# Optimization experiments

Measured on AMD Instinct MI355X. Metric: run time of the kernel, lower is better.

## Reference

```python
import jax, jax.numpy as jnp
import numpy as np
import math

EMBED_DIM = 1024
NUM_HEADS = 16
HEAD_DIM = EMBED_DIM // NUM_HEADS
ACT_BITS = 8
WGT_BITS = 8


def fake_quant(x, n_bits):
    # Per-tensor symmetric fake quantization with straight-through estimator.
    qmax = 2.0 ** (n_bits - 1) - 1.0  # 127 for 8 bits
    scale = jnp.maximum(jnp.max(jnp.abs(x)) / qmax, 1e-8)
    q = jnp.clip(jnp.round(x / scale), -qmax - 1.0, qmax) * scale
    return x + jax.lax.stop_gradient(q - x)


def setup_inputs() -> dict:
    key = jax.random.key(0)
    ks = jax.random.split(key, 7)
    S, B, D = 2048, 2, EMBED_DIM
    return {
        "query": jax.random.normal(ks[0], (S, B, D), dtype=jnp.float32),
        "key": jax.random.normal(ks[1], (S, B, D), dtype=jnp.float32),
        "value": jax.random.normal(ks[2], (S, B, D), dtype=jnp.float32),
        "Wi": jax.random.normal(ks[3], (3 * D, D), dtype=jnp.float32) * (1.0 / math.sqrt(D)),
        "bi": jax.random.normal(ks[4], (3 * D,), dtype=jnp.float32) * 0.01,
        "Wo": jax.random.normal(ks[5], (D, D), dtype=jnp.float32) * (1.0 / math.sqrt(D)),
        "bo": jax.random.normal(ks[6], (D,), dtype=jnp.float32) * 0.01,
    }


def reference(query, key, value, Wi, bi, Wo, bo):
    D, H, hd = EMBED_DIM, NUM_HEADS, HEAD_DIM
    len_q, batch, _ = query.shape
    len_k = key.shape[0]

    Wi_q = fake_quant(Wi, WGT_BITS)
    Wo_q = fake_quant(Wo, WGT_BITS)

    # in-projections (full 3D projection per input, then chunk, as in source)
    Xq = fake_quant(query @ Wi_q.T + bi, ACT_BITS)
    Xk = fake_quant(key @ Wi_q.T + bi, ACT_BITS)
    Xv = fake_quant(value @ Wi_q.T + bi, ACT_BITS)
    Q = Xq[..., :D]
    K = Xk[..., D:2 * D]
    V = Xv[..., 2 * D:]

    # [len, B, D] -> [B*H, len, hd]
    q = Q.reshape(len_q, batch * H, hd).transpose(1, 0, 2)
    k = K.reshape(len_k, batch * H, hd).transpose(1, 0, 2)
    v = V.reshape(len_k, batch * H, hd).transpose(1, 0, 2)

    q = fake_quant(q / math.sqrt(hd), ACT_BITS)
    attn = jnp.einsum('bqd,bkd->bqk', q, k)  # note: attn/softmax fake-quants in source are no-ops (result discarded)
    attn = jax.nn.softmax(attn, axis=-1)
    heads = fake_quant(jnp.einsum('bqk,bkd->bqd', attn, v), ACT_BITS)

    # [B*H, len_q, hd] -> [len_q*B, D]
    heads_reshape = heads.transpose(1, 0, 2).reshape(len_q * batch, D)
    y = (heads_reshape @ Wo_q.T + bo).reshape(len_q, batch, D)
    return fake_quant(y, ACT_BITS)
```

## Files before the change

kernel.cpp:

```cpp
#include <hip/hip_runtime.h>
#include <math.h>


typedef _Float16 f16;
typedef _Float16 half8 __attribute__((ext_vector_type(8)));
typedef _Float16 half4 __attribute__((ext_vector_type(4)));
typedef _Float16 half2v __attribute__((ext_vector_type(2)));
typedef __fp16 fp16x2 __attribute__((ext_vector_type(2)));
typedef float floatx4 __attribute__((ext_vector_type(4)));
typedef int int4v __attribute__((ext_vector_type(4)));

#define QMAX 127.0f

#define SLOT_WI 0
#define SLOT_WO 1
#define SLOT_XQ 2
#define SLOT_XK 3
#define SLOT_XV 4
#define SLOT_HD 5
#define SLOT_Y  6
#define SLOT_Q  7
#define SLOT_A  8

__device__ __forceinline__ float slot_scale(const unsigned* slots, int slot, float premul) {
  if (slot < 0) return 1.0f;
  return fmaxf(__uint_as_float(slots[slot]) * premul / QMAX, 1e-8f);
}

__device__ __forceinline__ float slot_scaleA(const unsigned* slots) {
  return fmaxf(__uint_as_float(slots[SLOT_A]) / 16256.0f, 1e-8f);
}

__device__ __forceinline__ void gl2lds16(const void* gsrc, void* ldst) {
  __builtin_amdgcn_global_load_lds((__attribute__((address_space(1))) void*)gsrc,
                                   (__attribute__((address_space(3))) void*)ldst, 16, 0, 0);
}

__device__ __forceinline__ half2v pack2(float a, float b) {
  fp16x2 r = __builtin_amdgcn_cvt_pkrtz(a, b);
  return __builtin_bit_cast(half2v, r);
}


__global__ __launch_bounds__(256) void absmax3_k(const float* __restrict__ Wi,
                                                 const float* __restrict__ Wo,
                                                 const float* __restrict__ q,
                                                 const float* __restrict__ k,
                                                 const float* __restrict__ v,
                                                 unsigned* __restrict__ slots) {
  __shared__ float red[256];
  int tid = threadIdx.x;
  int bid = blockIdx.x;
  const float4* x4;
  int n4, i0, stride, slot;
  if (bid < 768) {
    x4 = (const float4*)Wi; n4 = 786432; i0 = bid * 256 + tid;
    stride = 768 * 256; slot = SLOT_WI;
  } else if (bid < 1024) {
    x4 = (const float4*)Wo; n4 = 262144; i0 = (bid - 768) * 256 + tid;
    stride = 256 * 256; slot = SLOT_WO;
  } else {
    int r = bid - 1024;
    int t = r >> 9;
    x4 = (const float4*)(t == 0 ? q : (t == 1 ? k : v));
    n4 = 1048576; i0 = (r & 511) * 256 + tid;
    stride = 512 * 256; slot = SLOT_A;
  }
  float lmax = 0.f;
  for (int i = i0; i < n4; i += stride) {
    float4 vv = x4[i];
    lmax = fmaxf(lmax, fmaxf(fmaxf(fabsf(vv.x), fabsf(vv.y)), fmaxf(fabsf(vv.z), fabsf(vv.w))));
  }
  red[tid] = lmax; __syncthreads();
  for (int sh = 128; sh > 0; sh >>= 1) {
    if (tid < sh) red[tid] = fmaxf(red[tid], red[tid + sh]);
    __syncthreads();
  }
  if (tid == 0) atomicMax(&slots[slot], __float_as_uint(red[0]));
}

__global__ __launch_bounds__(256) void quantw_k(const float* __restrict__ Wi,
                                                const float* __restrict__ Wo,
                                                char* __restrict__ Wi8,
                                                char* __restrict__ Wo8,
                                                const unsigned* __restrict__ slots) {
  int j = blockIdx.x * 256 + threadIdx.x;
  const float* src; char* dst; float s; int a;
  if (j < 196608) {
    s = slot_scale(slots, SLOT_WI, 1.0f); src = Wi; dst = Wi8; a = j;
  } else {
    s = slot_scale(slots, SLOT_WO, 1.0f); src = Wo; dst = Wo8; a = j - 196608;
  }
  int m = ((a >> 10) << 4) | (a & 15);
  int k0 = ((((a >> 6) & 15) << 2) | ((a >> 4) & 3)) << 4;
  const float4* row = (const float4*)(src + (size_t)m * 1024 + k0);
  char ob[16] __attribute__((aligned(16)));
#pragma unroll
  for (int c = 0; c < 4; ++c) {
    float4 x = row[c];
    float xs[4] = {x.x, x.y, x.z, x.w};
#pragma unroll
    for (int u = 0; u < 4; ++u)
      ob[c * 4 + u] = (signed char)(int)fminf(fmaxf(rintf(xs[u] / s), -128.0f), 127.0f);
  }
  *(int4*)(dst + (size_t)a * 16) = *(const int4*)ob;
}

__global__ __launch_bounds__(256) void digitize_k(const float* __restrict__ q,
                                                  const float* __restrict__ k,
                                                  const float* __restrict__ v,
                                                  char* __restrict__ A1,
                                                  char* __restrict__ A2,
                                                  const unsigned* __restrict__ slots) {
  float inv = 1.0f / slot_scaleA(slots);
  int j = blockIdx.x * 256 + threadIdx.x;
  int t = j >> 18;
  int a = j & 262143;
  const float* src = (t == 0 ? q : (t == 1 ? k : v));
  int m = ((a >> 10) << 4) | (a & 15);
  int k0 = ((((a >> 6) & 15) << 2) | ((a >> 4) & 3)) << 4;
  const float4* row = (const float4*)(src + (size_t)m * 1024 + k0);
  char o1[16] __attribute__((aligned(16)));
  char o2[16] __attribute__((aligned(16)));
#pragma unroll
  for (int c = 0; c < 4; ++c) {
    float4 x = row[c];
    float xs[4] = {x.x, x.y, x.z, x.w};
#pragma unroll
    for (int u = 0; u < 4; ++u) {
      float qv = fminf(fmaxf(rintf(xs[u] * inv), -16256.0f), 16256.0f);
      float c1 = rintf(qv * 0.0078125f);
      o1[c * 4 + u] = (signed char)(int)c1;
      o2[c * 4 + u] = (signed char)(int)(qv - 128.0f * c1);
    }
  }
  size_t off = (size_t)t * 4194304 + (size_t)a * 16;
  *(int4*)(A1 + off) = *(const int4*)o1;
  *(int4*)(A2 + off) = *(const int4*)o2;
}

__global__ __launch_bounds__(256) void quantf_k(const float* __restrict__ in, float* __restrict__ out,
                                                int n4, unsigned* __restrict__ slots,
                                                int sSlot, float premul) {
  float s = slot_scale(slots, sSlot, premul);
  const float4* in4 = (const float4*)in;
  float4* out4 = (float4*)out;
  for (int i = blockIdx.x * 256 + threadIdx.x; i < n4; i += gridDim.x * 256) {
    float4 v = in4[i];
    float xs[4] = {v.x, v.y, v.z, v.w};
#pragma unroll
    for (int u = 0; u < 4; ++u) {
      float r = rintf((xs[u] * premul) / s);
      r = fminf(fmaxf(r, -128.0f), 127.0f);
      xs[u] = r * s;
    }
    out4[i] = make_float4(xs[0], xs[1], xs[2], xs[3]);
  }
}

__global__ __launch_bounds__(256) void quanti2_k(const float* __restrict__ Xk,
                                                 f16* __restrict__ Kint,
                                                 const float* __restrict__ Xq,
                                                 f16* __restrict__ Qc,
                                                 unsigned* __restrict__ slots) {
  __shared__ float red[256];
  bool isQ = blockIdx.x >= 1024;
  const float* in = isQ ? Xq : Xk;
  f16* out = isQ ? Qc : Kint;
  float s = slot_scale(slots, isQ ? SLOT_XQ : SLOT_XK, 1.0f);
  int b = isQ ? blockIdx.x - 1024 : blockIdx.x;
  float lmax = 0.f;
  const float4* in4 = (const float4*)in;
  for (int i = b * 256 + threadIdx.x; i < 1048576; i += 1024 * 256) {
    float4 v = in4[i];
    float xs[4] = {v.x, v.y, v.z, v.w};
    half4 o;
#pragma unroll
    for (int u = 0; u < 4; ++u) {
      float r = rintf(xs[u] / s);
      r = fminf(fmaxf(r, -128.0f), 127.0f);
      o[u] = (f16)r;
      lmax = fmaxf(lmax, fabsf(r));
    }
    *(half4*)(out + (size_t)i * 4) = o;
  }
  if (isQ) {
    int tid = threadIdx.x;
    red[tid] = lmax; __syncthreads();
    for (int sh = 128; sh > 0; sh >>= 1) {
      if (tid < sh) red[tid] = fmaxf(red[tid], red[tid + sh]);
      __syncthreads();
    }
    if (tid == 0) atomicMax(&slots[SLOT_Q], __float_as_uint(red[0] * s));
  }
}

__global__ __launch_bounds__(256) void quant8_k(const float* __restrict__ in, char* __restrict__ out,
                                                const unsigned* __restrict__ slots,
                                                int sSlot) {
  float s = slot_scale(slots, sSlot, 1.0f);
  int a = blockIdx.x * 256 + threadIdx.x;
  int m = ((a >> 10) << 4) | (a & 15);
  int k0 = ((((a >> 6) & 15) << 2) | ((a >> 4) & 3)) << 4;
  const float4* row = (const float4*)(in + (size_t)m * 1024 + k0);
  char ob[16] __attribute__((aligned(16)));
#pragma unroll
  for (int c = 0; c < 4; ++c) {
    float4 x = row[c];
    float xs[4] = {x.x, x.y, x.z, x.w};
#pragma unroll
    for (int u = 0; u < 4; ++u)
      ob[c * 4 + u] = (signed char)(int)fminf(fmaxf(rintf(xs[u] / s), -128.0f), 127.0f);
  }
  *(int4*)(out + (size_t)a * 16) = *(const int4*)ob;
}

__global__ __launch_bounds__(256) void quantv_t_k(const float* __restrict__ Xv,
                                                  f16* __restrict__ Vt,
                                                  const unsigned* __restrict__ slots) {
  __shared__ f16 T[64][68];
  int tid = threadIdx.x;
  int bh = blockIdx.y, b = bh >> 4, h = bh & 15;
  int k0 = blockIdx.x * 64;
  float s = slot_scale(slots, SLOT_XV, 1.0f);
#pragma unroll
  for (int it = 0; it < 4; ++it) {
    int idx = tid + it * 256;
    int row = idx >> 4, dseg = idx & 15;
    float4 v = *(const float4*)(Xv + ((size_t)(k0 + row) * 2 + b) * 1024 + h * 64 + dseg * 4);
    float xs[4] = {v.x, v.y, v.z, v.w};
    half4 o;
#pragma unroll
    for (int u = 0; u < 4; ++u) {
      float r = rintf(xs[u] / s);
      o[u] = (f16)fminf(fmaxf(r, -128.0f), 127.0f);
    }
    *(half4*)&T[row][dseg * 4] = o;
  }
  __syncthreads();
#pragma unroll
  for (int it = 0; it < 2; ++it) {
    int sdx = tid + it * 256;
    int d = sdx >> 3, j8 = sdx & 7;
    half8 o;
#pragma unroll
    for (int l = 0; l < 8; ++l) {
      int pos = j8 * 8 + l;
      int tp = pos >> 5, pq = (pos & 31) >> 3, jj = pos & 7;
      int k = tp * 32 + pq * 4 + ((jj < 4) ? jj : jj + 12);
      o[l] = T[k][d];
    }
    *(half8*)(Vt + ((size_t)bh * 64 + d) * 2048 + k0 + j8 * 8) = o;
  }
}

__global__ __launch_bounds__(512) void gemm_qkv_i8_k(const char* __restrict__ A1,
                                                     const char* __restrict__ A2,
                                                     const char* __restrict__ B8,
                                                     const float* __restrict__ bias,
                                                     float* __restrict__ Xout,
                                                     unsigned* __restrict__ slots) {
  __shared__ char As1[2][8192];
  __shared__ char As2[2][8192];
  __shared__ char Bs8[2][8192];
  float* red = (float*)&As1[0][0];

  int tid = threadIdx.x;
  int lane = tid & 63, w = tid >> 6;
  int wm = w >> 1, wn = w & 1;
  int quad = lane >> 4, l15 = lane & 15;
  int t = blockIdx.y >> 5;
  int m0 = (blockIdx.y & 31) * 128;
  int n0 = blockIdx.x * 128;
  size_t aoff = (size_t)t * 4194304;

  const char* a1p = A1 + aoff;
  const char* a2p = A2 + aoff;

  int4v acc1[2][4], acc2[2][4];
#pragma unroll
  for (int i = 0; i < 2; ++i)
#pragma unroll
    for (int j = 0; j < 4; ++j) {
      acc1[i][j] = (int4v){0, 0, 0, 0};
      acc2[i][j] = (int4v){0, 0, 0, 0};
    }

  auto stage = [&](int buf, int kk) __attribute__((always_inline)) {
    size_t ac = ((size_t)((m0 >> 4) + w) << 14) + ((kk >> 6) << 10) + lane * 16;
    size_t bc = ((size_t)((n0 >> 4) + w) << 14) + ((kk >> 6) << 10) + lane * 16;
    gl2lds16(a1p + ac, &As1[buf][w * 1024]);
    gl2lds16(a2p + ac, &As2[buf][w * 1024]);
    gl2lds16(B8 + bc, &Bs8[buf][w * 1024]);
  };

  auto compute = [&](int buf) __attribute__((always_inline)) {
    int4v bf[4];
#pragma unroll
    for (int j = 0; j < 4; ++j)
      bf[j] = *(const int4v*)&Bs8[buf][(wn * 4 + j) * 1024 + lane * 16];
    int4v a1f[2];
#pragma unroll
    for (int i = 0; i < 2; ++i)
      a1f[i] = *(const int4v*)&As1[buf][(wm * 2 + i) * 1024 + lane * 16];
#pragma unroll
    for (int i = 0; i < 2; ++i)
#pragma unroll
      for (int j = 0; j < 4; ++j)
        acc1[i][j] = __builtin_amdgcn_mfma_i32_16x16x64_i8(a1f[i], bf[j], acc1[i][j], 0, 0, 0);
    int4v a2f[2];
#pragma unroll
    for (int i = 0; i < 2; ++i)
      a2f[i] = *(const int4v*)&As2[buf][(wm * 2 + i) * 1024 + lane * 16];
#pragma unroll
    for (int i = 0; i < 2; ++i)
#pragma unroll
      for (int j = 0; j < 4; ++j)
        acc2[i][j] = __builtin_amdgcn_mfma_i32_16x16x64_i8(a2f[i], bf[j], acc2[i][j], 0, 0, 0);
  };

  stage(0, 0);
  __syncthreads();
  for (int kt = 0; kt < 7; ++kt) {
    stage(1, (2 * kt + 1) * 64);
    compute(0);
    __syncthreads();
    stage(0, (2 * kt + 2) * 64);
    compute(1);
    __syncthreads();
  }
  stage(1, 960);
  compute(0);
  __syncthreads();
  compute(1);

  float sc = slot_scaleA(slots) * slot_scale(slots, SLOT_WI, 1.0f);
  int colLo = t * 1024;
  float* outT = Xout + aoff;
  float lmax = 0.f;
#pragma unroll
  for (int i = 0; i < 2; ++i) {
#pragma unroll
    for (int j = 0; j < 4; ++j) {
      int gn = n0 + wn * 64 + j * 16 + l15;
      float bv = bias[gn];
      bool wr = (gn >= colLo && gn < colLo + 1024);
#pragma unroll
      for (int r = 0; r < 4; ++r) {
        int gm = m0 + wm * 32 + i * 16 + quad * 4 + r;
        float vv = fmaf((float)acc1[i][j][r], 128.0f, (float)acc2[i][j][r]) * sc + bv;
        lmax = fmaxf(lmax, fabsf(vv));
        if (wr) outT[(size_t)gm * 1024 + (gn - colLo)] = vv;
      }
    }
  }
  red[tid] = lmax; __syncthreads();
  for (int sh = 256; sh > 0; sh >>= 1) {
    if (tid < sh) red[tid] = fmaxf(red[tid], red[tid + sh]);
    __syncthreads();
  }
  if (tid == 0) atomicMax(&slots[SLOT_XQ + t], __float_as_uint(red[0]));
}

__global__ __launch_bounds__(512) void gemm_i8out_k(const char* __restrict__ A8,
                                                    const char* __restrict__ B8,
                                                    const float* __restrict__ bias,
                                                    float* __restrict__ out,
                                                    unsigned* __restrict__ slots) {
  __shared__ char As8[2][8192];
  __shared__ char Bs8[2][8192];
  float* red = (float*)&As8[0][0];

  int tid = threadIdx.x;
  int lane = tid & 63, w = tid >> 6;
  int wm = w >> 1, wn = w & 1;
  int quad = lane >> 4, l15 = lane & 15;
  int m0 = blockIdx.y * 128, n0 = blockIdx.x * 128;

  int4v acc[2][4];
#pragma unroll
  for (int i = 0; i < 2; ++i)
#pragma unroll
    for (int j = 0; j < 4; ++j) acc[i][j] = (int4v){0, 0, 0, 0};

  auto stage = [&](int buf, int kk) __attribute__((always_inline)) {
    size_t ac = ((size_t)((m0 >> 4) + w) << 14) + ((kk >> 6) << 10) + lane * 16;
    size_t bc = ((size_t)((n0 >> 4) + w) << 14) + ((kk >> 6) << 10) + lane * 16;
    gl2lds16(A8 + ac, &As8[buf][w * 1024]);
    gl2lds16(B8 + bc, &Bs8[buf][w * 1024]);
  };

  auto compute = [&](int buf) __attribute__((always_inline)) {
    int4v bf[4];
#pragma unroll
    for (int j = 0; j < 4; ++j)
      bf[j] = *(const int4v*)&Bs8[buf][(wn * 4 + j) * 1024 + lane * 16];
    int4v af[2];
#pragma unroll
    for (int i = 0; i < 2; ++i)
      af[i] = *(const int4v*)&As8[buf][(wm * 2 + i) * 1024 + lane * 16];
#pragma unroll
    for (int i = 0; i < 2; ++i)
#pragma unroll
      for (int j = 0; j < 4; ++j)
        acc[i][j] = __builtin_amdgcn_mfma_i32_16x16x64_i8(af[i], bf[j], acc[i][j], 0, 0, 0);
  };

  stage(0, 0);
  __syncthreads();
  for (int kt = 0; kt < 7; ++kt) {
    stage(1, (2 * kt + 1) * 64);
    compute(0);
    __syncthreads();
    stage(0, (2 * kt + 2) * 64);
    compute(1);
    __syncthreads();
  }
  stage(1, 960);
  compute(0);
  __syncthreads();
  compute(1);

  float sc = slot_scale(slots, SLOT_HD, 1.0f) * slot_scale(slots, SLOT_WO, 1.0f);
  float lmax = 0.f;
#pragma unroll
  for (int i = 0; i < 2; ++i) {
#pragma unroll
    for (int j = 0; j < 4; ++j) {
      int gn = n0 + wn * 64 + j * 16 + l15;
      float bv = bias[gn];
#pragma unroll
      for (int r = 0; r < 4; ++r) {
        int gm = m0 + wm * 32 + i * 16 + quad * 4 + r;
        float v = (float)acc[i][j][r] * sc + bv;
        lmax = fmaxf(lmax, fabsf(v));
        out[(size_t)gm * 1024 + gn] = v;
      }
    }
  }
  red[tid] = lmax; __syncthreads();
  for (int sh = 256; sh > 0; sh >>= 1) {
    if (tid < sh) red[tid] = fmaxf(red[tid], red[tid + sh]);
    __syncthreads();
  }
  if (tid == 0) atomicMax(&slots[SLOT_Y], __float_as_uint(red[0]));
}

__global__ __launch_bounds__(256) void attn_k(const f16* __restrict__ Qc,
                                              const f16* __restrict__ Kh,
                                              const f16* __restrict__ Vt,
                                              float* __restrict__ heads,
                                              unsigned* __restrict__ slots) {
  __shared__ f16 Ks[2][64 * 64];
  __shared__ f16 Vs[2][64][72];
  __shared__ float lred[4][2][16];
  __shared__ float red[256];

  int tid = threadIdx.x;
  int lane = tid & 63, w = tid >> 6;
  int quad = lane >> 4, l15 = lane & 15;
  int bh = blockIdx.y, b = bh >> 4, h = bh & 15;
  int q0 = blockIdx.x * 128;

  float s1 = slot_scale(slots, SLOT_XQ, 1.0f);
  float sq = slot_scale(slots, SLOT_Q, 0.125f);
  float sk = slot_scale(slots, SLOT_XK, 1.0f);
  float sv = slot_scale(slots, SLOT_XV, 1.0f);
  float cS = sq * sk * 1.44269504088896340736f;
  const float FOFF = 12.0f;

  half8 qf[2][2];
#pragma unroll
  for (int s = 0; s < 2; ++s) {
    const f16* qrow = Qc + ((size_t)(q0 + w * 32 + s * 16 + l15) * 2 + b) * 1024 + h * 64;
    half8 qr0 = *(const half8*)(qrow + quad * 8);
    half8 qr1 = *(const half8*)(qrow + 32 + quad * 8);
#pragma unroll
    for (int u = 0; u < 8; ++u) {
      float x0 = ((float)qr0[u] * s1) * 0.125f;
      float x1 = ((float)qr1[u] * s1) * 0.125f;
      qf[s][0][u] = (f16)fminf(fmaxf(rintf(x0 / sq), -128.0f), 127.0f);
      qf[s][1][u] = (f16)fminf(fmaxf(rintf(x1 / sq), -128.0f), 127.0f);
    }
  }

  int ksrow = lane >> 3;
  int ksp = lane & 7;
  int vr0 = tid >> 3, vs0 = (tid & 7) * 8;

  floatx4 oacc[2][4];
#pragma unroll
  for (int s = 0; s < 2; ++s)
#pragma unroll
    for (int d = 0; d < 4; ++d) oacc[s][d] = (floatx4){0.f, 0.f, 0.f, 0.f};
  float lsum[2] = {0.f, 0.f};

  const f16* vbase = Vt + (size_t)bh * 131072;
  half8 va, vb;

  auto stageK = [&](int bf, int kt) __attribute__((always_inline)) {
#pragma unroll
    for (int t = 0; t < 2; ++t) {
      int r0 = (w * 2 + t) * 8;
      int row = r0 + ksrow;
      int g = ksp ^ (row & 7);
      gl2lds16(Kh + ((size_t)(kt + row) * 2 + b) * 1024 + h * 64 + g * 8, &Ks[bf][r0 * 64]);
    }
  };
  auto loadV = [&](int kt) __attribute__((always_inline)) {
    va = *(const half8*)(vbase + (size_t)vr0 * 2048 + kt + vs0);
    vb = *(const half8*)(vbase + (size_t)(vr0 + 32) * 2048 + kt + vs0);
  };
  auto writeV = [&](int bf) __attribute__((always_inline)) {
    *(half8*)&Vs[bf][vr0][vs0] = va;
    *(half8*)&Vs[bf][vr0 + 32][vs0] = vb;
  };

  auto compute = [&](int bf) __attribute__((always_inline)) {
    half8 aph[2][2], apl[2][2];
#pragma unroll
    for (int t = 0; t < 4; ++t) {
      int row = t * 16 + l15;
      int g1 = quad ^ (row & 7);
      half8 kf0 = *(half8*)&Ks[bf][row * 64 + g1 * 8];
      half8 kf1 = *(half8*)&Ks[bf][row * 64 + (g1 ^ 4) * 8];
      int tp = t >> 1, hi = (t & 1) * 4;
#pragma unroll
      for (int s = 0; s < 2; ++s) {
        floatx4 sacc = (floatx4){0.f, 0.f, 0.f, 0.f};
        sacc = __builtin_amdgcn_mfma_f32_16x16x32_f16(kf0, qf[s][0], sacc, 0, 0, 0);
        sacc = __builtin_amdgcn_mfma_f32_16x16x32_f16(kf1, qf[s][1], sacc, 0, 0, 0);
        float p0 = __builtin_amdgcn_exp2f(fmaf(sacc[0], cS, -FOFF));
        float p1 = __builtin_amdgcn_exp2f(fmaf(sacc[1], cS, -FOFF));
        float p2 = __builtin_amdgcn_exp2f(fmaf(sacc[2], cS, -FOFF));
        float p3 = __builtin_amdgcn_exp2f(fmaf(sacc[3], cS, -FOFF));
        lsum[s] += (p0 + p1) + (p2 + p3);
        half2v h01 = pack2(p0, p1);
        half2v h23 = pack2(p2, p3);
        half2v l01 = pack2(p0 - (float)h01[0], p1 - (float)h01[1]);
        half2v l23 = pack2(p2 - (float)h23[0], p3 - (float)h23[1]);
        aph[s][tp][hi + 0] = h01[0]; aph[s][tp][hi + 1] = h01[1];
        aph[s][tp][hi + 2] = h23[0]; aph[s][tp][hi + 3] = h23[1];
        apl[s][tp][hi + 0] = l01[0]; apl[s][tp][hi + 1] = l01[1];
        apl[s][tp][hi + 2] = l23[0]; apl[s][tp][hi + 3] = l23[1];
      }
    }

#pragma unroll
    for (int d = 0; d < 4; ++d) {
      const f16* vsrow = &Vs[bf][d * 16 + l15][0];
      half8 b0 = *(const half8*)(vsrow + quad * 8);
      half8 b1 = *(const half8*)(vsrow + 32 + quad * 8);
#pragma unroll
      for (int s = 0; s < 2; ++s) {
        oacc[s][d] = __builtin_amdgcn_mfma_f32_16x16x32_f16(aph[s][0], b0, oacc[s][d], 0, 0, 0);
        oacc[s][d] = __builtin_amdgcn_mfma_f32_16x16x32_f16(apl[s][0], b0, oacc[s][d], 0, 0, 0);
        oacc[s][d] = __builtin_amdgcn_mfma_f32_16x16x32_f16(aph[s][1], b1, oacc[s][d], 0, 0, 0);
        oacc[s][d] = __builtin_amdgcn_mfma_f32_16x16x32_f16(apl[s][1], b1, oacc[s][d], 0, 0, 0);
      }
    }
  };

  stageK(0, 0);
  loadV(0);
  writeV(0);
  loadV(64);
  __syncthreads();

  int buf = 0;
  for (int it = 0; it < 31; ++it) {
    stageK(buf ^ 1, (it + 1) * 64);
    writeV(buf ^ 1);
    if (it < 30) loadV((it + 2) * 64);
    compute(buf);
    __syncthreads();
    buf ^= 1;
  }
  compute(buf);

#pragma unroll
  for (int s = 0; s < 2; ++s) {
    float l = lsum[s];
    l += __shfl_xor(l, 16);
    l += __shfl_xor(l, 32);
    lred[w][s][l15] = l;
  }
  float linv[2][4];
#pragma unroll
  for (int s = 0; s < 2; ++s)
#pragma unroll
    for (int r = 0; r < 4; ++r) linv[s][r] = sv / lred[w][s][quad * 4 + r];

  float lmax = 0.f;
#pragma unroll
  for (int s = 0; s < 2; ++s)
#pragma unroll
    for (int d = 0; d < 4; ++d)
#pragma unroll
      for (int r = 0; r < 4; ++r) {
        float hv = oacc[s][d][r] * linv[s][r];
        heads[((size_t)(q0 + w * 32 + s * 16 + quad * 4 + r) * 2 + b) * 1024 +
              h * 64 + d * 16 + l15] = hv;
        lmax = fmaxf(lmax, fabsf(hv));
      }
  red[tid] = lmax; __syncthreads();
  for (int sh = 128; sh > 0; sh >>= 1) {
    if (tid < sh) red[tid] = fmaxf(red[tid], red[tid + sh]);
    __syncthreads();
  }
  if (tid == 0) atomicMax(&slots[SLOT_HD], __float_as_uint(red[0]));
}

extern "C" void kernel_launch(void* const* d_in, const int* in_sizes, int n_in,
                              void* d_out, int out_size, void* d_ws, size_t ws_size,
                              hipStream_t stream) {
  (void)in_sizes; (void)n_in; (void)out_size; (void)ws_size;
  const float* query = (const float*)d_in[0];
  const float* key   = (const float*)d_in[1];
  const float* value = (const float*)d_in[2];
  const float* Wi    = (const float*)d_in[3];
  const float* bi    = (const float*)d_in[4];
  const float* Wo    = (const float*)d_in[5];
  const float* bo    = (const float*)d_in[6];
  float* out = (float*)d_out;

  char* p = (char*)d_ws;
  unsigned* slots = (unsigned*)p;            p += 1024;
  char* Wi8 = p;                             p += 3072 * 1024;
  char* Wo8 = p;                             p += 1024 * 1024;
  char* A1  = p;                             p += 12288 * 1024;
  char* A2  = p;                             p += 12288 * 1024;
  float* Hd = (float*)A1;
  f16* Kint = (f16*)(A2 + 4194304);
  float* Xq = (float*)p;                     p += 4096 * 1024 * 4;
  float* Y  = Xq;
  float* Xk = (float*)p;                     p += 4096 * 1024 * 4;
  f16* Qc   = (f16*)Xk;
  float* Xv = (float*)p;                     p += 4096 * 1024 * 4;
  char* Hint8 = (char*)Xv + 4096 * 1024 * 2;
  f16* Vt   = (f16*)p;                       p += 4096 * 1024 * 2;

  hipMemsetAsync(slots, 0, 64, stream);
  absmax3_k<<<2560, 256, 0, stream>>>(Wi, Wo, query, key, value, slots);
  quantw_k<<<1024, 256, 0, stream>>>(Wi, Wo, Wi8, Wo8, slots);
  digitize_k<<<3072, 256, 0, stream>>>(query, key, value, A1, A2, slots);

  dim3 gq(24, 96);
  gemm_qkv_i8_k<<<gq, 512, 0, stream>>>(A1, A2, Wi8, bi, Xq, slots);

  quanti2_k<<<2048, 256, 0, stream>>>(Xk, Kint, Xq, Qc, slots);

  dim3 gvt(32, 32);
  quantv_t_k<<<gvt, 256, 0, stream>>>(Xv, Vt, slots);

  dim3 ga(16, 32);
  attn_k<<<ga, 256, 0, stream>>>(Qc, Kint, Vt, Hd, slots);

  quant8_k<<<1024, 256, 0, stream>>>(Hd, Hint8, slots, SLOT_HD);

  dim3 g2(8, 32);
  gemm_i8out_k<<<g2, 512, 0, stream>>>(Hint8, Wo8, bo, Y, slots);

  quantf_k<<<1024, 256, 0, stream>>>(Y, out, 1048576, slots, SLOT_Y, 1.0f);
}
```

Baseline: 359.1 us.

## Merge elementwise prep/post kernels and load GEMM B fragments directly from global

```diff
diff --git a/kernel.cpp b/kernel.cpp
--- a/kernel.cpp
+++ b/kernel.cpp
@@ -79,64 +79,65 @@
   if (tid == 0) atomicMax(&slots[slot], __float_as_uint(red[0]));
 }
 
-__global__ __launch_bounds__(256) void quantw_k(const float* __restrict__ Wi,
-                                                const float* __restrict__ Wo,
-                                                char* __restrict__ Wi8,
-                                                char* __restrict__ Wo8,
-                                                const unsigned* __restrict__ slots) {
-  int j = blockIdx.x * 256 + threadIdx.x;
-  const float* src; char* dst; float s; int a;
-  if (j < 196608) {
-    s = slot_scale(slots, SLOT_WI, 1.0f); src = Wi; dst = Wi8; a = j;
+__global__ __launch_bounds__(256) void prep_k(const float* __restrict__ Wi,
+                                              const float* __restrict__ Wo,
+                                              const float* __restrict__ q,
+                                              const float* __restrict__ k,
+                                              const float* __restrict__ v,
+                                              char* __restrict__ Wi8,
+                                              char* __restrict__ Wo8,
+                                              char* __restrict__ A1,
+                                              char* __restrict__ A2,
+                                              const unsigned* __restrict__ slots) {
+  int bid = blockIdx.x;
+  if (bid < 1024) {
+    int j = bid * 256 + threadIdx.x;
+    const float* src; char* dst; float s; int a;
+    if (j < 196608) {
+      s = slot_scale(slots, SLOT_WI, 1.0f); src = Wi; dst = Wi8; a = j;
+    } else {
+      s = slot_scale(slots, SLOT_WO, 1.0f); src = Wo; dst = Wo8; a = j - 196608;
+    }
+    int m = ((a >> 10) << 4) | (a & 15);
+    int k0 = ((((a >> 6) & 15) << 2) | ((a >> 4) & 3)) << 4;
+    const float4* row = (const float4*)(src + (size_t)m * 1024 + k0);
+    char ob[16] __attribute__((aligned(16)));
+#pragma unroll
+    for (int c = 0; c < 4; ++c) {
+      float4 x = row[c];
+      float xs[4] = {x.x, x.y, x.z, x.w};
+#pragma unroll
+      for (int u = 0; u < 4; ++u)
+        ob[c * 4 + u] = (signed char)(int)fminf(fmaxf(rintf(xs[u] / s), -128.0f), 127.0f);
+    }
+    *(int4*)(dst + (size_t)a * 16) = *(const int4*)ob;
   } else {
-    s = slot_scale(slots, SLOT_WO, 1.0f); src = Wo; dst = Wo8; a = j - 196608;
-  }
-  int m = ((a >> 10) << 4) | (a & 15);
-  int k0 = ((((a >> 6) & 15) << 2) | ((a >> 4) & 3)) << 4;
-  const float4* row = (const float4*)(src + (size_t)m * 1024 + k0);
-  char ob[16] __attribute__((aligned(16)));
-#pragma unroll
-  for (int c = 0; c < 4; ++c) {
-    float4 x = row[c];
-    float xs[4] = {x.x, x.y, x.z, x.w};
-#pragma unroll
-    for (int u = 0; u < 4; ++u)
-      ob[c * 4 + u] = (signed char)(int)fminf(fmaxf(rintf(xs[u] / s), -128.0f), 127.0f);
-  }
-  *(int4*)(dst + (size_t)a * 16) = *(const int4*)ob;
-}
-
-__global__ __launch_bounds__(256) void digitize_k(const float* __restrict__ q,
-                                                  const float* __restrict__ k,
-                                                  const float* __restrict__ v,
-                                                  char* __restrict__ A1,
-                                                  char* __restrict__ A2,
-                                                  const unsigned* __restrict__ slots) {
-  float inv = 1.0f / slot_scaleA(slots);
-  int j = blockIdx.x * 256 + threadIdx.x;
-  int t = j >> 18;
-  int a = j & 262143;
-  const float* src = (t == 0 ? q : (t == 1 ? k : v));
-  int m = ((a >> 10) << 4) | (a & 15);
-  int k0 = ((((a >> 6) & 15) << 2) | ((a >> 4) & 3)) << 4;
-  const float4* row = (const float4*)(src + (size_t)m * 1024 + k0);
-  char o1[16] __attribute__((aligned(16)));
-  char o2[16] __attribute__((aligned(16)));
-#pragma unroll
-  for (int c = 0; c < 4; ++c) {
-    float4 x = row[c];
-    float xs[4] = {x.x, x.y, x.z, x.w};
-#pragma unroll
-    for (int u = 0; u < 4; ++u) {
-      float qv = fminf(fmaxf(rintf(xs[u] * inv), -16256.0f), 16256.0f);
-      float c1 = rintf(qv * 0.0078125f);
-      o1[c * 4 + u] = (signed char)(int)c1;
-      o2[c * 4 + u] = (signed char)(int)(qv - 128.0f * c1);
-    }
-  }
-  size_t off = (size_t)t * 4194304 + (size_t)a * 16;
-  *(int4*)(A1 + off) = *(const int4*)o1;
-  *(int4*)(A2 + off) = *(const int4*)o2;
+    float inv = 1.0f / slot_scaleA(slots);
+    int j = (bid - 1024) * 256 + threadIdx.x;
+    int t = j >> 18;
+    int a = j & 262143;
+    const float* src = (t == 0 ? q : (t == 1 ? k : v));
+    int m = ((a >> 10) << 4) | (a & 15);
+    int k0 = ((((a >> 6) & 15) << 2) | ((a >> 4) & 3)) << 4;
+    const float4* row = (const float4*)(src + (size_t)m * 1024 + k0);
+    char o1[16] __attribute__((aligned(16)));
+    char o2[16] __attribute__((aligned(16)));
+#pragma unroll
+    for (int c = 0; c < 4; ++c) {
+      float4 x = row[c];
+      float xs[4] = {x.x, x.y, x.z, x.w};
+#pragma unroll
+      for (int u = 0; u < 4; ++u) {
+        float qv = fminf(fmaxf(rintf(xs[u] * inv), -16256.0f), 16256.0f);
+        float c1 = rintf(qv * 0.0078125f);
+        o1[c * 4 + u] = (signed char)(int)c1;
+        o2[c * 4 + u] = (signed char)(int)(qv - 128.0f * c1);
+      }
+    }
+    size_t off = (size_t)t * 4194304 + (size_t)a * 16;
+    *(int4*)(A1 + off) = *(const int4*)o1;
+    *(int4*)(A2 + off) = *(const int4*)o2;
+  }
 }
 
 __global__ __launch_bounds__(256) void quantf_k(const float* __restrict__ in, float* __restrict__ out,
@@ -158,40 +159,80 @@
   }
 }
 
-__global__ __launch_bounds__(256) void quanti2_k(const float* __restrict__ Xk,
-                                                 f16* __restrict__ Kint,
-                                                 const float* __restrict__ Xq,
-                                                 f16* __restrict__ Qc,
-                                                 unsigned* __restrict__ slots) {
+__global__ __launch_bounds__(256) void post_k(const float* __restrict__ Xk,
+                                              f16* __restrict__ Kint,
+                                              const float* __restrict__ Xq,
+                                              f16* __restrict__ Qc,
+                                              const float* __restrict__ Xv,
+                                              f16* __restrict__ Vt,
+                                              unsigned* __restrict__ slots) {
   __shared__ float red[256];
-  bool isQ = blockIdx.x >= 1024;
-  const float* in = isQ ? Xq : Xk;
-  f16* out = isQ ? Qc : Kint;
-  float s = slot_scale(slots, isQ ? SLOT_XQ : SLOT_XK, 1.0f);
-  int b = isQ ? blockIdx.x - 1024 : blockIdx.x;
-  float lmax = 0.f;
-  const float4* in4 = (const float4*)in;
-  for (int i = b * 256 + threadIdx.x; i < 1048576; i += 1024 * 256) {
-    float4 v = in4[i];
-    float xs[4] = {v.x, v.y, v.z, v.w};
-    half4 o;
-#pragma unroll
-    for (int u = 0; u < 4; ++u) {
-      float r = rintf(xs[u] / s);
-      r = fminf(fmaxf(r, -128.0f), 127.0f);
-      o[u] = (f16)r;
-      lmax = fmaxf(lmax, fabsf(r));
-    }
-    *(half4*)(out + (size_t)i * 4) = o;
-  }
-  if (isQ) {
-    int tid = threadIdx.x;
-    red[tid] = lmax; __syncthreads();
-    for (int sh = 128; sh > 0; sh >>= 1) {
-      if (tid < sh) red[tid] = fmaxf(red[tid], red[tid + sh]);
-      __syncthreads();
-    }
-    if (tid == 0) atomicMax(&slots[SLOT_Q], __float_as_uint(red[0] * s));
+  __shared__ f16 T[64][68];
+  int tid = threadIdx.x;
+  int bid = blockIdx.x;
+  if (bid < 2048) {
+    bool isQ = bid >= 1024;
+    const float* in = isQ ? Xq : Xk;
+    f16* out = isQ ? Qc : Kint;
+    float s = slot_scale(slots, isQ ? SLOT_XQ : SLOT_XK, 1.0f);
+    int b = isQ ? bid - 1024 : bid;
+    float lmax = 0.f;
+    const float4* in4 = (const float4*)in;
+    for (int i = b * 256 + tid; i < 1048576; i += 1024 * 256) {
+      float4 v = in4[i];
+      float xs[4] = {v.x, v.y, v.z, v.w};
+      half4 o;
+#pragma unroll
+      for (int u = 0; u < 4; ++u) {
+        float r = rintf(xs[u] / s);
+        r = fminf(fmaxf(r, -128.0f), 127.0f);
+        o[u] = (f16)r;
+        lmax = fmaxf(lmax, fabsf(r));
+      }
+      *(half4*)(out + (size_t)i * 4) = o;
+    }
+    if (isQ) {
+      red[tid] = lmax; __syncthreads();
+      for (int sh = 128; sh > 0; sh >>= 1) {
+        if (tid < sh) red[tid] = fmaxf(red[tid], red[tid + sh]);
+        __syncthreads();
+      }
+      if (tid == 0) atomicMax(&slots[SLOT_Q], __float_as_uint(red[0] * s));
+    }
+  } else {
+    int vt = bid - 2048;
+    int bh = vt >> 5, b = bh >> 4, h = bh & 15;
+    int k0 = (vt & 31) * 64;
+    float s = slot_scale(slots, SLOT_XV, 1.0f);
+#pragma unroll
+    for (int it = 0; it < 4; ++it) {
+      int idx = tid + it * 256;
+      int row = idx >> 4, dseg = idx & 15;
+      float4 v = *(const float4*)(Xv + ((size_t)(k0 + row) * 2 + b) * 1024 + h * 64 + dseg * 4);
+      float xs[4] = {v.x, v.y, v.z, v.w};
+      half4 o;
+#pragma unroll
+      for (int u = 0; u < 4; ++u) {
+        float r = rintf(xs[u] / s);
+        o[u] = (f16)fminf(fmaxf(r, -128.0f), 127.0f);
+      }
+      *(half4*)&T[row][dseg * 4] = o;
+    }
+    __syncthreads();
+#pragma unroll
+    for (int it = 0; it < 2; ++it) {
+      int sdx = tid + it * 256;
+      int d = sdx >> 3, j8 = sdx & 7;
+      half8 o;
+#pragma unroll
+      for (int l = 0; l < 8; ++l) {
+        int pos = j8 * 8 + l;
+        int tp = pos >> 5, pq = (pos & 31) >> 3, jj = pos & 7;
+        int k = tp * 32 + pq * 4 + ((jj < 4) ? jj : jj + 12);
+        o[l] = T[k][d];
+      }
+      *(half8*)(Vt + ((size_t)bh * 64 + d) * 2048 + k0 + j8 * 8) = o;
+    }
   }
 }
 
@@ -215,45 +256,6 @@
   *(int4*)(out + (size_t)a * 16) = *(const int4*)ob;
 }
 
-__global__ __launch_bounds__(256) void quantv_t_k(const float* __restrict__ Xv,
-                                                  f16* __restrict__ Vt,
-                                                  const unsigned* __restrict__ slots) {
-  __shared__ f16 T[64][68];
-  int tid = threadIdx.x;
-  int bh = blockIdx.y, b = bh >> 4, h = bh & 15;
-  int k0 = blockIdx.x * 64;
-  float s = slot_scale(slots, SLOT_XV, 1.0f);
-#pragma unroll
-  for (int it = 0; it < 4; ++it) {
-    int idx = tid + it * 256;
-    int row = idx >> 4, dseg = idx & 15;
-    float4 v = *(const float4*)(Xv + ((size_t)(k0 + row) * 2 + b) * 1024 + h * 64 + dseg * 4);
-    float xs[4] = {v.x, v.y, v.z, v.w};
-    half4 o;
-#pragma unroll
-    for (int u = 0; u < 4; ++u) {
-      float r = rintf(xs[u] / s);
-      o[u] = (f16)fminf(fmaxf(r, -128.0f), 127.0f);
-    }
-    *(half4*)&T[row][dseg * 4] = o;
-  }
-  __syncthreads();
-#pragma unroll
-  for (int it = 0; it < 2; ++it) {
-    int sdx = tid + it * 256;
-    int d = sdx >> 3, j8 = sdx & 7;
-    half8 o;
-#pragma unroll
-    for (int l = 0; l < 8; ++l) {
-      int pos = j8 * 8 + l;
-      int tp = pos >> 5, pq = (pos & 31) >> 3, jj = pos & 7;
-      int k = tp * 32 + pq * 4 + ((jj < 4) ? jj : jj + 12);
-      o[l] = T[k][d];
-    }
-    *(half8*)(Vt + ((size_t)bh * 64 + d) * 2048 + k0 + j8 * 8) = o;
-  }
-}
-
 __global__ __launch_bounds__(512) void gemm_qkv_i8_k(const char* __restrict__ A1,
                                                      const char* __restrict__ A2,
                                                      const char* __restrict__ B8,
@@ -262,7 +264,6 @@
                                                      unsigned* __restrict__ slots) {
   __shared__ char As1[2][8192];
   __shared__ char As2[2][8192];
-  __shared__ char Bs8[2][8192];
   float* red = (float*)&As1[0][0];
 
   int tid = threadIdx.x;
@@ -288,17 +289,18 @@
 
   auto stage = [&](int buf, int kk) __attribute__((always_inline)) {
     size_t ac = ((size_t)((m0 >> 4) + w) << 14) + ((kk >> 6) << 10) + lane * 16;
-    size_t bc = ((size_t)((n0 >> 4) + w) << 14) + ((kk >> 6) << 10) + lane * 16;
     gl2lds16(a1p + ac, &As1[buf][w * 1024]);
     gl2lds16(a2p + ac, &As2[buf][w * 1024]);
-    gl2lds16(B8 + bc, &Bs8[buf][w * 1024]);
-  };
-
-  auto compute = [&](int buf) __attribute__((always_inline)) {
-    int4v bf[4];
+  };
+
+  auto loadB = [&](int kk, int4v* bf) __attribute__((always_inline)) {
 #pragma unroll
     for (int j = 0; j < 4; ++j)
-      bf[j] = *(const int4v*)&Bs8[buf][(wn * 4 + j) * 1024 + lane * 16];
+      bf[j] = *(const int4v*)(B8 + ((size_t)((n0 >> 4) + wn * 4 + j) << 14) +
+                              (size_t)((kk >> 6) << 10) + lane * 16);
+  };
+
+  auto computeA = [&](int buf, const int4v* bf) __attribute__((always_inline)) {
     int4v a1f[2];
 #pragma unroll
     for (int i = 0; i < 2; ++i)
@@ -322,17 +324,25 @@
   stage(0, 0);
   __syncthreads();
   for (int kt = 0; kt < 7; ++kt) {
+    int4v bf[4];
+    loadB((2 * kt) * 64, bf);
     stage(1, (2 * kt + 1) * 64);
-    compute(0);
-    __syncthreads();
+    computeA(0, bf);
+    __syncthreads();
+    loadB((2 * kt + 1) * 64, bf);
     stage(0, (2 * kt + 2) * 64);
-    compute(1);
-    __syncthreads();
-  }
-  stage(1, 960);
-  compute(0);
-  __syncthreads();
-  compute(1);
+    computeA(1, bf);
+    __syncthreads();
+  }
+  {
+    int4v bf[4];
+    loadB(896, bf);
+    stage(1, 960);
+    computeA(0, bf);
+    __syncthreads();
+    loadB(960, bf);
+    computeA(1, bf);
+  }
 
   float sc = slot_scaleA(slots) * slot_scale(slots, SLOT_WI, 1.0f);
   int colLo = t * 1024;
@@ -368,7 +378,6 @@
                                                     float* __restrict__ out,
                                                     unsigned* __restrict__ slots) {
   __shared__ char As8[2][8192];
-  __shared__ char Bs8[2][8192];
   float* red = (float*)&As8[0][0];
 
   int tid = threadIdx.x;
@@ -385,16 +394,17 @@
 
   auto stage = [&](int buf, int kk) __attribute__((always_inline)) {
     size_t ac = ((size_t)((m0 >> 4) + w) << 14) + ((kk >> 6) << 10) + lane * 16;
-    size_t bc = ((size_t)((n0 >> 4) + w) << 14) + ((kk >> 6) << 10) + lane * 16;
     gl2lds16(A8 + ac, &As8[buf][w * 1024]);
-    gl2lds16(B8 + bc, &Bs8[buf][w * 1024]);
-  };
-
-  auto compute = [&](int buf) __attribute__((always_inline)) {
-    int4v bf[4];
+  };
+
+  auto loadB = [&](int kk, int4v* bf) __attribute__((always_inline)) {
 #pragma unroll
     for (int j = 0; j < 4; ++j)
-      bf[j] = *(const int4v*)&Bs8[buf][(wn * 4 + j) * 1024 + lane * 16];
+      bf[j] = *(const int4v*)(B8 + ((size_t)((n0 >> 4) + wn * 4 + j) << 14) +
+                              (size_t)((kk >> 6) << 10) + lane * 16);
+  };
+
+  auto computeA = [&](int buf, const int4v* bf) __attribute__((always_inline)) {
     int4v af[2];
 #pragma unroll
     for (int i = 0; i < 2; ++i)
@@ -409,17 +419,25 @@
   stage(0, 0);
   __syncthreads();
   for (int kt = 0; kt < 7; ++kt) {
+    int4v bf[4];
+    loadB((2 * kt) * 64, bf);
     stage(1, (2 * kt + 1) * 64);
-    compute(0);
-    __syncthreads();
+    computeA(0, bf);
+    __syncthreads();
+    loadB((2 * kt + 1) * 64, bf);
     stage(0, (2 * kt + 2) * 64);
-    compute(1);
-    __syncthreads();
-  }
-  stage(1, 960);
-  compute(0);
-  __syncthreads();
-  compute(1);
+    computeA(1, bf);
+    __syncthreads();
+  }
+  {
+    int4v bf[4];
+    loadB(896, bf);
+    stage(1, 960);
+    computeA(0, bf);
+    __syncthreads();
+    loadB(960, bf);
+    computeA(1, bf);
+  }
 
   float sc = slot_scale(slots, SLOT_HD, 1.0f) * slot_scale(slots, SLOT_WO, 1.0f);
   float lmax = 0.f;
@@ -642,16 +660,12 @@
 
   hipMemsetAsync(slots, 0, 64, stream);
   absmax3_k<<<2560, 256, 0, stream>>>(Wi, Wo, query, key, value, slots);
-  quantw_k<<<1024, 256, 0, stream>>>(Wi, Wo, Wi8, Wo8, slots);
-  digitize_k<<<3072, 256, 0, stream>>>(query, key, value, A1, A2, slots);
+  prep_k<<<4096, 256, 0, stream>>>(Wi, Wo, query, key, value, Wi8, Wo8, A1, A2, slots);
 
   dim3 gq(24, 96);
   gemm_qkv_i8_k<<<gq, 512, 0, stream>>>(A1, A2, Wi8, bi, Xq, slots);
 
-  quanti2_k<<<2048, 256, 0, stream>>>(Xk, Kint, Xq, Qc, slots);
-
-  dim3 gvt(32, 32);
-  quantv_t_k<<<gvt, 256, 0, stream>>>(Xv, Vt, slots);
+  post_k<<<3072, 256, 0, stream>>>(Xk, Kint, Xq, Qc, Xv, Vt, slots);
 
   dim3 ga(16, 32);
   attn_k<<<ga, 256, 0, stream>>>(Qc, Kint, Vt, Hd, slots);
```

Result: slower. 366.5 us (+2.1%).
